# Kernel tuning notes

Hardware: AMD Instinct MI355X
Metric: run time of the kernel (lower is better)

## Reference

```python
import jax, jax.numpy as jnp
import numpy as np
import math

N_EMBD = 1024
N_HEAD = 16

def setup_inputs() -> dict:
    key = jax.random.key(0)
    ks = jax.random.split(key, 5)
    C = N_EMBD
    x = jax.random.normal(ks[0], (4, 2048, C), dtype=jnp.float32)
    # params (torch Linear: y = x @ W.T + b)
    w_attn = jax.random.normal(ks[1], (3 * C, C), dtype=jnp.float32) * (1.0 / math.sqrt(C))
    b_attn = jnp.zeros((3 * C,), dtype=jnp.float32)
    w_proj = jax.random.normal(ks[2], (C, C), dtype=jnp.float32) * (1.0 / math.sqrt(C))
    b_proj = jnp.zeros((C,), dtype=jnp.float32)
    return {"x": x, "w_attn": w_attn, "b_attn": b_attn, "w_proj": w_proj, "b_proj": b_proj}


def reference(x, w_attn, b_attn, w_proj, b_proj):
    B, T, C = x.shape
    H = N_HEAD
    hd = C // H
    qkv = x @ w_attn.T + b_attn  # [B,T,3C]
    q, k, v = jnp.split(qkv, 3, axis=2)
    # [B,H,T,hd]
    q = q.reshape(B, T, H, hd).transpose(0, 2, 1, 3)
    k = k.reshape(B, T, H, hd).transpose(0, 2, 1, 3)
    v = v.reshape(B, T, H, hd).transpose(0, 2, 1, 3)
    att = jnp.einsum('bhqd,bhkd->bhqk', q, k) * (1.0 / math.sqrt(hd))
    causal = jnp.tril(jnp.ones((T, T), dtype=bool))
    att = jnp.where(causal, att, jnp.float32(-jnp.inf))
    att = jax.nn.softmax(att, axis=-1)
    y = jnp.einsum('bhqk,bhkd->bhqd', att, v)
    y = y.transpose(0, 2, 1, 3).reshape(B, T, C)
    return y @ w_proj.T + b_proj
```

## Files before the change

kernel.cpp:

```cpp
#include <hip/hip_runtime.h>
#include <hip/hip_bf16.h>
#include <stdint.h>

using bf16 = __hip_bfloat16;
typedef __attribute__((ext_vector_type(4))) float f32x4;
typedef __attribute__((ext_vector_type(8))) short s16x8;
typedef __attribute__((ext_vector_type(4))) short s16x4;

#define MFMA_B16(a, b, c)   __builtin_amdgcn_mfma_f32_16x16x32_bf16((a), (b), (c), 0, 0, 0)
#define MFMA16_B16(a, b, c) __builtin_amdgcn_mfma_f32_16x16x16bf16_1k((a), (b), (c), 0, 0, 0)

__device__ __forceinline__ void gld_lds16(const bf16* g, bf16* l) {
  __builtin_amdgcn_global_load_lds(
      (const __attribute__((address_space(1))) uint32_t*)g,
      (__attribute__((address_space(3))) uint32_t*)l, 16, 0, 0);
}

__device__ __forceinline__ short bf16r(float f) {
  uint32_t u = __float_as_uint(f);
  return (short)((u + 0x7FFFu + ((u >> 16) & 1u)) >> 16);
}
__device__ __forceinline__ float bf4f(short s) {
  return __uint_as_float(((uint32_t)(unsigned short)s) << 16);
}

constexpr int MT = 8192;
constexpr int KT = 1024;
constexpr size_t Q_OFF  = 0;
constexpr size_t K_OFF  = 8388608;
constexpr size_t VT_OFF = 16777216;
constexpr size_t Y_OFF  = 25165824;
constexpr size_t XB_OFF = 33554432;
constexpr size_t WA_OFF = 41943040;
constexpr size_t WP_OFF = 45088768;
constexpr size_t BA_OFF = 46137344;
constexpr size_t BP_OFF = 46140416;
constexpr size_t FLAG_W = 23070720;
constexpr size_t WS_NEED_BYTES = 23070721ull * 4ull;

__device__ __forceinline__ int inputs_are_f32(const uint32_t* __restrict__ x) {
  int hits = 0;
  for (int i = 0; i < 256; ++i) {
    uint32_t lo = x[i] & 0x7FFFu;
    hits += (lo >= 12288u && lo < 17408u) ? 1 : 0;
  }
  return hits < 128;
}

__device__ __forceinline__ uint32_t f32pair_to_bf16(float f0, float f1) {
  uint32_t u0 = __float_as_uint(f0), u1 = __float_as_uint(f1);
  uint32_t h0 = (u0 + 0x7FFFu + ((u0 >> 16) & 1u)) >> 16;
  uint32_t h1 = (u1 + 0x7FFFu + ((u1 >> 16) & 1u)) >> 16;
  return (h0 & 0xFFFFu) | (h1 << 16);
}

__global__ void convert_inputs(const uint32_t* __restrict__ x, const uint32_t* __restrict__ wa,
                               const uint32_t* __restrict__ ba, const uint32_t* __restrict__ wp,
                               const uint32_t* __restrict__ bp, uint32_t* __restrict__ ws) {
  __shared__ int sflag;
  if (threadIdx.x == 0) {
    sflag = inputs_are_f32(x);
    if (blockIdx.x == 0) ws[FLAG_W] = (uint32_t)sflag;
  }
  __syncthreads();
  const int f32f = sflag;
  const size_t total4 = 6293504 / 4;
  for (size_t i4 = (size_t)blockIdx.x * blockDim.x + threadIdx.x; i4 < total4;
       i4 += (size_t)gridDim.x * blockDim.x) {
    const size_t i = i4 * 4;
    const uint32_t* src; size_t j, dst;
    if (i < 4194304)      { src = x;  j = i;           dst = 16777216 + j; }
    else if (i < 5767168) { src = wa; j = i - 4194304; dst = 20971520 + j; }
    else if (i < 5768704) { src = ba; j = i - 5767168; dst = 23068672 + j; }
    else if (i < 6292992) { src = wp; j = i - 5768704; dst = 22544384 + j; }
    else                  { src = bp; j = i - 6292992; dst = 23070208 + j; }
    uint4 w;
    if (f32f) {
      const float* fs = (const float*)src + 2 * j;
      const uint4 a = *(const uint4*)(fs);
      const uint4 b = *(const uint4*)(fs + 4);
      w.x = f32pair_to_bf16(__uint_as_float(a.x), __uint_as_float(a.y));
      w.y = f32pair_to_bf16(__uint_as_float(a.z), __uint_as_float(a.w));
      w.z = f32pair_to_bf16(__uint_as_float(b.x), __uint_as_float(b.y));
      w.w = f32pair_to_bf16(__uint_as_float(b.z), __uint_as_float(b.w));
    } else {
      w = *(const uint4*)(src + j);
    }
    *(uint4*)(ws + dst) = w;
  }
}

template <int MODE, int N>
__device__ __forceinline__ void gemm_body(const bf16* __restrict__ A, const bf16* __restrict__ W,
                                          const bf16* __restrict__ bias, bf16* __restrict__ outb,
                                          const uint32_t* __restrict__ flagp,
                                          void* __restrict__ outv) {
  const int tid  = threadIdx.x;
  const int wave = tid >> 6, lane = tid & 63;
  const int quad = lane >> 4, l16 = lane & 15;
  const int wm = wave & 1, wn = wave >> 1;
  constexpr int NBX = N / 128, NWG = NBX * (MT / 128);
  const int dsp = blockIdx.y * NBX + blockIdx.x;
  const int wg  = (dsp & 7) * (NWG >> 3) + (dsp >> 3);
  const int m0 = (wg / NBX) * 128, n0 = (wg % NBX) * 128;
  const bool swapd = (MODE == 0) || (n0 < 2048);

  __shared__ __align__(16) bf16 As[2][2][128][32];
  __shared__ __align__(16) bf16 Bs[2][2][128][32];

  const int f32o = (MODE == 0 && flagp != nullptr) ? (int)flagp[0] : 0;

  const f32x4 fz = {0.f, 0.f, 0.f, 0.f};
  f32x4 acc[4][4];
#pragma unroll
  for (int i = 0; i < 4; ++i)
#pragma unroll
    for (int j = 0; j < 4; ++j) acc[i][j] = fz;

  const bf16* Ab = A + (size_t)m0 * KT;
  const bf16* Wb = W + (size_t)n0 * KT;
  int crow[4], coff[4];
#pragma unroll
  for (int j = 0; j < 4; ++j) {
    const int c = j * 256 + tid;
    crow[j] = (c >> 2) & 127;
    coff[j] = (c >> 9) * 32 + ((c & 3) ^ ((c >> 3) & 3)) * 8;
  }
  const int ksw = (l16 >> 1) & 3;

  auto stage = [&](int d, int kt) {
    const int k0 = kt * 64;
#pragma unroll
    for (int j = 0; j < 4; ++j) {
      const int c = j * 256 + tid;
      gld_lds16(Ab + (size_t)crow[j] * KT + k0 + coff[j], (bf16*)As + d * 8192 + c * 8);
      gld_lds16(Wb + (size_t)crow[j] * KT + k0 + coff[j], (bf16*)Bs + d * 8192 + c * 8);
    }
  };

  stage(0, 0);
#pragma unroll 1
  for (int kt = 0; kt < KT / 64; ++kt) {
    const int cur = kt & 1;
    asm volatile("s_waitcnt lgkmcnt(0)" ::: "memory");
    __builtin_amdgcn_s_barrier();
    if (kt + 1 < KT / 64) {
      stage(cur ^ 1, kt + 1);
      asm volatile("s_waitcnt vmcnt(8)" ::: "memory");
    } else {
      asm volatile("s_waitcnt vmcnt(0)" ::: "memory");
    }
    __builtin_amdgcn_s_barrier();

#pragma unroll
    for (int ks = 0; ks < 2; ++ks) {
      s16x8 af[4], bf_[4];
#pragma unroll
      for (int i = 0; i < 4; ++i)
        af[i] = *(const s16x8*)(&As[cur][ks][wm * 64 + i * 16 + l16][(quad ^ ksw) * 8]);
#pragma unroll
      for (int j = 0; j < 4; ++j)
        bf_[j] = *(const s16x8*)(&Bs[cur][ks][wn * 64 + j * 16 + l16][(quad ^ ksw) * 8]);
      if (swapd) {
#pragma unroll
        for (int j = 0; j < 4; ++j)
#pragma unroll
          for (int i = 0; i < 4; ++i)
            acc[j][i] = MFMA_B16(bf_[j], af[i], acc[j][i]);
      } else {
#pragma unroll
        for (int i = 0; i < 4; ++i)
#pragma unroll
          for (int j = 0; j < 4; ++j)
            acc[i][j] = MFMA_B16(af[i], bf_[j], acc[i][j]);
      }
    }
  }

  if (MODE == 0) {
#pragma unroll
    for (int j = 0; j < 4; ++j) {
      const int cb = n0 + wn * 64 + j * 16 + quad * 4;
      const s16x4 b4 = *(const s16x4*)(bias + cb);
#pragma unroll
      for (int i = 0; i < 4; ++i) {
        const int t = m0 + wm * 64 + i * 16 + l16;
        if (f32o) {
          f32x4 v;
#pragma unroll
          for (int r = 0; r < 4; ++r) v[r] = acc[j][i][r] + bf4f(b4[r]);
          *(f32x4*)((float*)outv + (size_t)t * N + cb) = v;
        } else {
          s16x4 o;
#pragma unroll
          for (int r = 0; r < 4; ++r) o[r] = bf16r(acc[j][i][r] + bf4f(b4[r]));
          *(s16x4*)((bf16*)outv + (size_t)t * N + cb) = o;
        }
      }
    }
  } else if (swapd) {
#pragma unroll
    for (int j = 0; j < 4; ++j) {
      const int nb = n0 + wn * 64 + j * 16 + quad * 4;
      const int which = nb >> 10, cc = nb & 1023;
      const int h = cc >> 6, d0 = cc & 63;
      const s16x4 b4 = *(const s16x4*)(bias + nb);
      bf16* segp = outb + (which ? K_OFF : Q_OFF);
#pragma unroll
      for (int i = 0; i < 4; ++i) {
        const int t = m0 + wm * 64 + i * 16 + l16;
        const int b_ = t >> 11, tt = t & 2047;
        s16x4 o;
#pragma unroll
        for (int r = 0; r < 4; ++r) o[r] = bf16r(acc[j][i][r] + bf4f(b4[r]));
        *(s16x4*)(segp + ((size_t)(b_ * 16 + h) * 2048 + tt) * 64 + d0) = o;
      }
    }
  } else {
#pragma unroll
    for (int j = 0; j < 4; ++j) {
      const int n = n0 + wn * 64 + j * 16 + l16;
      const int h = (n & 1023) >> 6, d = n & 63;
      const float bv = __bfloat162float(bias[n]);
#pragma unroll
      for (int i = 0; i < 4; ++i) {
        const int t0 = m0 + wm * 64 + i * 16 + quad * 4;
        const int b_ = t0 >> 11, tt0 = t0 & 2047;
        const int tts = (tt0 & ~31) | (((((tt0 >> 2) & 7) ^ (d & 7))) << 2);
        s16x4 o;
#pragma unroll
        for (int r = 0; r < 4; ++r) o[r] = bf16r(acc[i][j][r] + bv);
        *(s16x4*)(outb + VT_OFF + ((size_t)(b_ * 16 + h) * 64 + d) * 2048 + tts) = o;
      }
    }
  }
}

__launch_bounds__(256, 2)
__global__ void gemm_qkv(const bf16* __restrict__ A, const bf16* __restrict__ W,
                         const bf16* __restrict__ bias, bf16* __restrict__ outb) {
  gemm_body<1, 3072>(A, W, bias, outb, nullptr, nullptr);
}

__launch_bounds__(256, 2)
__global__ void gemm_proj(const bf16* __restrict__ A, const bf16* __restrict__ W,
                          const bf16* __restrict__ bias,
                          const uint32_t* __restrict__ flagp, void* __restrict__ outv) {
  gemm_body<0, 1024>(A, W, bias, nullptr, flagp, outv);
}

__launch_bounds__(256, 4)
__global__ void attn_fused(const bf16* __restrict__ qw, const bf16* __restrict__ kw,
                           const bf16* __restrict__ vtw, bf16* __restrict__ yw) {
  const int tid  = threadIdx.x;
  const int wave = tid >> 6, lane = tid & 63;
  const int quad = lane >> 4, l16 = lane & 15;
  const int dsp = blockIdx.x;
  const int wg  = (dsp & 7) * 128 + (dsp >> 3);
  const int ic  = wg & 127;
  const int s   = ic >> 3;
  const int qt  = (s < 4) ? (15 - s) : (s < 8) ? (s - 4) : (s < 12) ? (19 - s) : (s - 8);
  const int bh  = (wg >> 7) * 8 + (ic & 7);
  const int b = bh >> 4, h = bh & 15;

  __shared__ __align__(16) bf16 Ks[2][2][64][32];
  __shared__ __align__(16) bf16 Vt[2][2][64][32];

  const bf16* Qb = qw + (size_t)bh * 2048 * 64;
  const bf16* Kb = kw + (size_t)bh * 2048 * 64;
  const bf16* Vb = vtw + (size_t)bh * 64 * 2048;

  const f32x4 fz = {0.f, 0.f, 0.f, 0.f};
  const float C1 = 0.18033688011112042f;
  const float C0 = -23.083120654223414f;
  s16x4 ones4;
#pragma unroll
  for (int i = 0; i < 4; ++i) ones4[i] = (short)0x3F80;

  const int c0 = wave * 128 + lane, c1 = c0 + 64;
  const int p0 = c0 >> 8, r0 = (c0 >> 2) & 63, s0 = c0 & 3;
  const int p1 = c1 >> 8, r1 = (c1 >> 2) & 63, s1 = c1 & 3;
  const int koff0 = p0 * 32 + (s0 ^ ((r0 >> 1) & 3)) * 8;
  const int koff1 = p1 * 32 + (s1 ^ ((r1 >> 1) & 3)) * 8;
  const int ksw = (l16 >> 1) & 3;

  const int q0 = qt * 128;
  const int qr0 = q0 + wave * 32;
  const int ntiles = qt * 2 + 2;

  s16x8 qf[2][2];
#pragma unroll
  for (int g = 0; g < 2; ++g)
#pragma unroll
    for (int ks = 0; ks < 2; ++ks)
      qf[g][ks] = *(const s16x8*)(Qb + (size_t)(qr0 + g * 16 + l16) * 64 +
                                  ks * 32 + quad * 8);

  f32x4 ot[2][4];
  f32x4 lacc[2];
#pragma unroll
  for (int g = 0; g < 2; ++g) {
#pragma unroll
    for (int dj = 0; dj < 4; ++dj) ot[g][dj] = fz;
    lacc[g] = fz;
  }

  gld_lds16(Kb + (size_t)r0 * 64 + koff0, (bf16*)Ks[0] + c0 * 8);
  gld_lds16(Kb + (size_t)r1 * 64 + koff1, (bf16*)Ks[0] + c1 * 8);
  gld_lds16(Vb + (size_t)r0 * 2048 + p0 * 32 + s0 * 8, (bf16*)Vt[0] + c0 * 8);
  gld_lds16(Vb + (size_t)r1 * 2048 + p1 * 32 + s1 * 8, (bf16*)Vt[0] + c1 * 8);

#pragma unroll 1
  for (int kt = 0; kt < ntiles; ++kt) {
    const int cur = kt & 1, nxt = cur ^ 1;
    __syncthreads();
    if (kt + 1 < ntiles) {
      const int kn = (kt + 1) * 64;
      gld_lds16(Kb + (size_t)(kn + r0) * 64 + koff0, (bf16*)Ks[nxt] + c0 * 8);
      gld_lds16(Kb + (size_t)(kn + r1) * 64 + koff1, (bf16*)Ks[nxt] + c1 * 8);
      gld_lds16(Vb + (size_t)r0 * 2048 + kn + p0 * 32 + s0 * 8, (bf16*)Vt[nxt] + c0 * 8);
      gld_lds16(Vb + (size_t)r1 * 2048 + kn + p1 * 32 + s1 * 8, (bf16*)Vt[nxt] + c1 * 8);
    }
    const int k0 = kt * 64;
    if (k0 <= qr0 + 31) {
      const bool diag = (k0 + 63 > qr0);
#pragma unroll
      for (int m4 = 0; m4 < 4; ++m4) {
        s16x8 kf0 = *(const s16x8*)(&Ks[cur][0][m4 * 16 + l16][(quad ^ ksw) * 8]);
        s16x8 kf1 = *(const s16x8*)(&Ks[cur][1][m4 * 16 + l16][(quad ^ ksw) * 8]);
        f32x4 st0 = fz, st1 = fz;
        __builtin_amdgcn_s_setprio(1);
        st0 = MFMA_B16(kf0, qf[0][0], st0);
        st0 = MFMA_B16(kf1, qf[0][1], st0);
        st1 = MFMA_B16(kf0, qf[1][0], st1);
        st1 = MFMA_B16(kf1, qf[1][1], st1);
        __builtin_amdgcn_s_setprio(0);

        s16x4 pb0, pb1;
        const int krow = k0 + m4 * 16 + quad * 4;
#pragma unroll
        for (int r = 0; r < 4; ++r) {
          float t0 = __builtin_fmaf(st0[r], C1, C0);
          float t1 = __builtin_fmaf(st1[r], C1, C0);
          if (diag) {
            if (krow + r > qr0 + l16) t0 = -512.0f;
            if (krow + r > qr0 + 16 + l16) t1 = -512.0f;
          }
          pb0[r] = (short)(__float_as_uint(__builtin_amdgcn_exp2f(t0)) >> 16);
          pb1[r] = (short)(__float_as_uint(__builtin_amdgcn_exp2f(t1)) >> 16);
        }
        __builtin_amdgcn_s_setprio(1);
        lacc[0] = MFMA16_B16(ones4, pb0, lacc[0]);
        lacc[1] = MFMA16_B16(ones4, pb1, lacc[1]);

        const int pan = m4 >> 1;
        const int cl = (m4 & 1) * 4 + quad;
#pragma unroll
        for (int dj = 0; dj < 4; ++dj) {
          s16x4 vf = *(const s16x4*)(&Vt[cur][pan][dj * 16 + l16][(cl ^ (l16 & 7)) * 4]);
          ot[0][dj] = MFMA16_B16(vf, pb0, ot[0][dj]);
          ot[1][dj] = MFMA16_B16(vf, pb1, ot[1][dj]);
        }
        __builtin_amdgcn_s_setprio(0);
      }
    }
  }
  __syncthreads();

#pragma unroll
  for (int g = 0; g < 2; ++g) {
    const int qrow = qr0 + g * 16 + l16;
    const float inv = 1.0f / lacc[g][0];
    bf16* dst = yw + ((size_t)(b * 2048 + qrow) * 16 + h) * 64;
#pragma unroll
    for (int dj = 0; dj < 4; ++dj) {
      s16x4 o4;
#pragma unroll
      for (int r = 0; r < 4; ++r) o4[r] = bf16r(ot[g][dj][r] * inv);
      *(s16x4*)(dst + dj * 16 + quad * 4) = o4;
    }
  }
}

extern "C" void kernel_launch(void* const* d_in, const int* in_sizes, int n_in,
                              void* d_out, int out_size, void* d_ws, size_t ws_size,
                              hipStream_t stream) {
  bf16* ws = (bf16*)d_ws;
  const bool have_cvt = ws_size >= WS_NEED_BYTES;

  const bf16 *xb, *wab, *bab, *wpb, *bpb;
  const uint32_t* flagp = nullptr;
  if (have_cvt) {
    convert_inputs<<<2048, 256, 0, stream>>>(
        (const uint32_t*)d_in[0], (const uint32_t*)d_in[1], (const uint32_t*)d_in[2],
        (const uint32_t*)d_in[3], (const uint32_t*)d_in[4], (uint32_t*)d_ws);
    xb = ws + XB_OFF; wab = ws + WA_OFF; bab = ws + BA_OFF;
    wpb = ws + WP_OFF; bpb = ws + BP_OFF;
    flagp = ((const uint32_t*)d_ws) + FLAG_W;
  } else {
    xb = (const bf16*)d_in[0]; wab = (const bf16*)d_in[1]; bab = (const bf16*)d_in[2];
    wpb = (const bf16*)d_in[3]; bpb = (const bf16*)d_in[4];
  }

  gemm_qkv<<<dim3(3072 / 128, MT / 128), 256, 0, stream>>>(xb, wab, bab, ws);
  attn_fused<<<dim3(1024), 256, 0, stream>>>(ws + Q_OFF, ws + K_OFF, ws + VT_OFF, ws + Y_OFF);
  gemm_proj<<<dim3(1024 / 128, MT / 128), 256, 0, stream>>>(ws + Y_OFF, wpb, bpb, flagp, d_out);
}
```

Before: 252.9 us.

## Enlarge QKV GEMM tile to 256x256 with 512-thread workgroups

```diff
diff --git a/kernel.cpp b/kernel.cpp
--- a/kernel.cpp
+++ b/kernel.cpp
@@ -90,30 +90,26 @@
   }
 }
 
-template <int MODE, int N>
-__device__ __forceinline__ void gemm_body(const bf16* __restrict__ A, const bf16* __restrict__ W,
-                                          const bf16* __restrict__ bias, bf16* __restrict__ outb,
-                                          const uint32_t* __restrict__ flagp,
-                                          void* __restrict__ outv) {
+__launch_bounds__(512, 2)
+__global__ void gemm_qkv(const bf16* __restrict__ A, const bf16* __restrict__ W,
+                         const bf16* __restrict__ bias, bf16* __restrict__ outb) {
   const int tid  = threadIdx.x;
   const int wave = tid >> 6, lane = tid & 63;
   const int quad = lane >> 4, l16 = lane & 15;
   const int wm = wave & 1, wn = wave >> 1;
-  constexpr int NBX = N / 128, NWG = NBX * (MT / 128);
+  constexpr int NBX = 3072 / 256, NWG = NBX * (MT / 256);
   const int dsp = blockIdx.y * NBX + blockIdx.x;
   const int wg  = (dsp & 7) * (NWG >> 3) + (dsp >> 3);
-  const int m0 = (wg / NBX) * 128, n0 = (wg % NBX) * 128;
-  const bool swapd = (MODE == 0) || (n0 < 2048);
-
-  __shared__ __align__(16) bf16 As[2][2][128][32];
-  __shared__ __align__(16) bf16 Bs[2][2][128][32];
-
-  const int f32o = (MODE == 0 && flagp != nullptr) ? (int)flagp[0] : 0;
+  const int m0 = (wg / NBX) * 256, n0 = (wg % NBX) * 256;
+  const bool swapd = (n0 < 2048);
+
+  __shared__ __align__(16) bf16 As[2][2][256][32];
+  __shared__ __align__(16) bf16 Bs[2][2][256][32];
 
   const f32x4 fz = {0.f, 0.f, 0.f, 0.f};
-  f32x4 acc[4][4];
-#pragma unroll
-  for (int i = 0; i < 4; ++i)
+  f32x4 acc[8][4];
+#pragma unroll
+  for (int i = 0; i < 8; ++i)
 #pragma unroll
     for (int j = 0; j < 4; ++j) acc[i][j] = fz;
 
@@ -122,9 +118,9 @@
   int crow[4], coff[4];
 #pragma unroll
   for (int j = 0; j < 4; ++j) {
-    const int c = j * 256 + tid;
-    crow[j] = (c >> 2) & 127;
-    coff[j] = (c >> 9) * 32 + ((c & 3) ^ ((c >> 3) & 3)) * 8;
+    const int c = j * 512 + tid;
+    crow[j] = (c >> 2) & 255;
+    coff[j] = (c >> 10) * 32 + ((c & 3) ^ ((c >> 3) & 3)) * 8;
   }
   const int ksw = (l16 >> 1) & 3;
 
@@ -132,9 +128,9 @@
     const int k0 = kt * 64;
 #pragma unroll
     for (int j = 0; j < 4; ++j) {
-      const int c = j * 256 + tid;
-      gld_lds16(Ab + (size_t)crow[j] * KT + k0 + coff[j], (bf16*)As + d * 8192 + c * 8);
-      gld_lds16(Wb + (size_t)crow[j] * KT + k0 + coff[j], (bf16*)Bs + d * 8192 + c * 8);
+      const int c = j * 512 + tid;
+      gld_lds16(Ab + (size_t)crow[j] * KT + k0 + coff[j], (bf16*)As + d * 16384 + c * 8);
+      gld_lds16(Wb + (size_t)crow[j] * KT + k0 + coff[j], (bf16*)Bs + d * 16384 + c * 8);
     }
   };
 
@@ -154,22 +150,22 @@
 
 #pragma unroll
     for (int ks = 0; ks < 2; ++ks) {
-      s16x8 af[4], bf_[4];
-#pragma unroll
-      for (int i = 0; i < 4; ++i)
-        af[i] = *(const s16x8*)(&As[cur][ks][wm * 64 + i * 16 + l16][(quad ^ ksw) * 8]);
+      s16x8 af[8], bf_[4];
+#pragma unroll
+      for (int i = 0; i < 8; ++i)
+        af[i] = *(const s16x8*)(&As[cur][ks][wm * 128 + i * 16 + l16][(quad ^ ksw) * 8]);
 #pragma unroll
       for (int j = 0; j < 4; ++j)
         bf_[j] = *(const s16x8*)(&Bs[cur][ks][wn * 64 + j * 16 + l16][(quad ^ ksw) * 8]);
       if (swapd) {
 #pragma unroll
-        for (int j = 0; j < 4; ++j)
-#pragma unroll
-          for (int i = 0; i < 4; ++i)
-            acc[j][i] = MFMA_B16(bf_[j], af[i], acc[j][i]);
+        for (int i = 0; i < 8; ++i)
+#pragma unroll
+          for (int j = 0; j < 4; ++j)
+            acc[i][j] = MFMA_B16(bf_[j], af[i], acc[i][j]);
       } else {
 #pragma unroll
-        for (int i = 0; i < 4; ++i)
+        for (int i = 0; i < 8; ++i)
 #pragma unroll
           for (int j = 0; j < 4; ++j)
             acc[i][j] = MFMA_B16(af[i], bf_[j], acc[i][j]);
@@ -177,28 +173,7 @@
     }
   }
 
-  if (MODE == 0) {
-#pragma unroll
-    for (int j = 0; j < 4; ++j) {
-      const int cb = n0 + wn * 64 + j * 16 + quad * 4;
-      const s16x4 b4 = *(const s16x4*)(bias + cb);
-#pragma unroll
-      for (int i = 0; i < 4; ++i) {
-        const int t = m0 + wm * 64 + i * 16 + l16;
-        if (f32o) {
-          f32x4 v;
-#pragma unroll
-          for (int r = 0; r < 4; ++r) v[r] = acc[j][i][r] + bf4f(b4[r]);
-          *(f32x4*)((float*)outv + (size_t)t * N + cb) = v;
-        } else {
-          s16x4 o;
-#pragma unroll
-          for (int r = 0; r < 4; ++r) o[r] = bf16r(acc[j][i][r] + bf4f(b4[r]));
-          *(s16x4*)((bf16*)outv + (size_t)t * N + cb) = o;
-        }
-      }
-    }
-  } else if (swapd) {
+  if (swapd) {
 #pragma unroll
     for (int j = 0; j < 4; ++j) {
       const int nb = n0 + wn * 64 + j * 16 + quad * 4;
@@ -207,12 +182,12 @@
       const s16x4 b4 = *(const s16x4*)(bias + nb);
       bf16* segp = outb + (which ? K_OFF : Q_OFF);
 #pragma unroll
-      for (int i = 0; i < 4; ++i) {
-        const int t = m0 + wm * 64 + i * 16 + l16;
+      for (int i = 0; i < 8; ++i) {
+        const int t = m0 + wm * 128 + i * 16 + l16;
         const int b_ = t >> 11, tt = t & 2047;
         s16x4 o;
 #pragma unroll
-        for (int r = 0; r < 4; ++r) o[r] = bf16r(acc[j][i][r] + bf4f(b4[r]));
+        for (int r = 0; r < 4; ++r) o[r] = bf16r(acc[i][j][r] + bf4f(b4[r]));
         *(s16x4*)(segp + ((size_t)(b_ * 16 + h) * 2048 + tt) * 64 + d0) = o;
       }
     }
@@ -223,8 +198,8 @@
       const int h = (n & 1023) >> 6, d = n & 63;
       const float bv = __bfloat162float(bias[n]);
 #pragma unroll
-      for (int i = 0; i < 4; ++i) {
-        const int t0 = m0 + wm * 64 + i * 16 + quad * 4;
+      for (int i = 0; i < 8; ++i) {
+        const int t0 = m0 + wm * 128 + i * 16 + quad * 4;
         const int b_ = t0 >> 11, tt0 = t0 & 2047;
         const int tts = (tt0 & ~31) | (((((tt0 >> 2) & 7) ^ (d & 7))) << 2);
         s16x4 o;
@@ -234,19 +209,106 @@
       }
     }
   }
-}
-
-__launch_bounds__(256, 2)
-__global__ void gemm_qkv(const bf16* __restrict__ A, const bf16* __restrict__ W,
-                         const bf16* __restrict__ bias, bf16* __restrict__ outb) {
-  gemm_body<1, 3072>(A, W, bias, outb, nullptr, nullptr);
 }
 
 __launch_bounds__(256, 2)
 __global__ void gemm_proj(const bf16* __restrict__ A, const bf16* __restrict__ W,
                           const bf16* __restrict__ bias,
                           const uint32_t* __restrict__ flagp, void* __restrict__ outv) {
-  gemm_body<0, 1024>(A, W, bias, nullptr, flagp, outv);
+  const int tid  = threadIdx.x;
+  const int wave = tid >> 6, lane = tid & 63;
+  const int quad = lane >> 4, l16 = lane & 15;
+  const int wm = wave & 1, wn = wave >> 1;
+  constexpr int N = 1024;
+  constexpr int NBX = N / 128, NWG = NBX * (MT / 128);
+  const int dsp = blockIdx.y * NBX + blockIdx.x;
+  const int wg  = (dsp & 7) * (NWG >> 3) + (dsp >> 3);
+  const int m0 = (wg / NBX) * 128, n0 = (wg % NBX) * 128;
+
+  __shared__ __align__(16) bf16 As[2][2][128][32];
+  __shared__ __align__(16) bf16 Bs[2][2][128][32];
+
+  const int f32o = (flagp != nullptr) ? (int)flagp[0] : 0;
+
+  const f32x4 fz = {0.f, 0.f, 0.f, 0.f};
+  f32x4 acc[4][4];
+#pragma unroll
+  for (int i = 0; i < 4; ++i)
+#pragma unroll
+    for (int j = 0; j < 4; ++j) acc[i][j] = fz;
+
+  const bf16* Ab = A + (size_t)m0 * KT;
+  const bf16* Wb = W + (size_t)n0 * KT;
+  int crow[4], coff[4];
+#pragma unroll
+  for (int j = 0; j < 4; ++j) {
+    const int c = j * 256 + tid;
+    crow[j] = (c >> 2) & 127;
+    coff[j] = (c >> 9) * 32 + ((c & 3) ^ ((c >> 3) & 3)) * 8;
+  }
+  const int ksw = (l16 >> 1) & 3;
+
+  auto stage = [&](int d, int kt) {
+    const int k0 = kt * 64;
+#pragma unroll
+    for (int j = 0; j < 4; ++j) {
+      const int c = j * 256 + tid;
+      gld_lds16(Ab + (size_t)crow[j] * KT + k0 + coff[j], (bf16*)As + d * 8192 + c * 8);
+      gld_lds16(Wb + (size_t)crow[j] * KT + k0 + coff[j], (bf16*)Bs + d * 8192 + c * 8);
+    }
+  };
+
+  stage(0, 0);
+#pragma unroll 1
+  for (int kt = 0; kt < KT / 64; ++kt) {
+    const int cur = kt & 1;
+    asm volatile("s_waitcnt lgkmcnt(0)" ::: "memory");
+    __builtin_amdgcn_s_barrier();
+    if (kt + 1 < KT / 64) {
+      stage(cur ^ 1, kt + 1);
+      asm volatile("s_waitcnt vmcnt(8)" ::: "memory");
+    } else {
+      asm volatile("s_waitcnt vmcnt(0)" ::: "memory");
+    }
+    __builtin_amdgcn_s_barrier();
+
+#pragma unroll
+    for (int ks = 0; ks < 2; ++ks) {
+      s16x8 af[4], bf_[4];
+#pragma unroll
+      for (int i = 0; i < 4; ++i)
+        af[i] = *(const s16x8*)(&As[cur][ks][wm * 64 + i * 16 + l16][(quad ^ ksw) * 8]);
+#pragma unroll
+      for (int j = 0; j < 4; ++j)
+        bf_[j] = *(const s16x8*)(&Bs[cur][ks][wn * 64 + j * 16 + l16][(quad ^ ksw) * 8]);
+#pragma unroll
+      for (int j = 0; j < 4; ++j)
+#pragma unroll
+        for (int i = 0; i < 4; ++i)
+          acc[j][i] = MFMA_B16(bf_[j], af[i], acc[j][i]);
+    }
+  }
+
+#pragma unroll
+  for (int j = 0; j < 4; ++j) {
+    const int cb = n0 + wn * 64 + j * 16 + quad * 4;
+    const s16x4 b4 = *(const s16x4*)(bias + cb);
+#pragma unroll
+    for (int i = 0; i < 4; ++i) {
+      const int t = m0 + wm * 64 + i * 16 + l16;
+      if (f32o) {
+        f32x4 v;
+#pragma unroll
+        for (int r = 0; r < 4; ++r) v[r] = acc[j][i][r] + bf4f(b4[r]);
+        *(f32x4*)((float*)outv + (size_t)t * N + cb) = v;
+      } else {
+        s16x4 o;
+#pragma unroll
+        for (int r = 0; r < 4; ++r) o[r] = bf16r(acc[j][i][r] + bf4f(b4[r]));
+        *(s16x4*)((bf16*)outv + (size_t)t * N + cb) = o;
+      }
+    }
+  }
 }
 
 __launch_bounds__(256, 4)
@@ -402,7 +464,7 @@
     wpb = (const bf16*)d_in[3]; bpb = (const bf16*)d_in[4];
   }
 
-  gemm_qkv<<<dim3(3072 / 128, MT / 128), 256, 0, stream>>>(xb, wab, bab, ws);
+  gemm_qkv<<<dim3(3072 / 256, MT / 256), 512, 0, stream>>>(xb, wab, bab, ws);
   attn_fused<<<dim3(1024), 256, 0, stream>>>(ws + Q_OFF, ws + K_OFF, ws + VT_OFF, ws + Y_OFF);
   gemm_proj<<<dim3(1024 / 128, MT / 128), 256, 0, stream>>>(ws + Y_OFF, wpb, bpb, flagp, d_out);
 }
```

New measurement: 554.7 us. 2.19x slower.
